# Performance work log

Hardware: AMD Instinct MI355X
Metric: run time of the kernel (lower is better)

## Reference

```python
import jax, jax.numpy as jnp
import numpy as np

NUM_GROUPS = 32
EPS = 1e-6


def setup_inputs() -> dict:
    key = jax.random.key(0)
    ks = jax.random.split(key, 11)
    b, c, h, w = 4, 512, 64, 64
    s = 0.02
    return {
        "x": jax.random.normal(ks[0], (b, c, h, w), dtype=jnp.float32),
        "gn_w": jnp.ones((c,), dtype=jnp.float32),
        "gn_b": jnp.zeros((c,), dtype=jnp.float32),
        "wq": jax.random.normal(ks[1], (c, c), dtype=jnp.float32) * s,
        "bq": jax.random.normal(ks[2], (c,), dtype=jnp.float32) * s,
        "wk": jax.random.normal(ks[3], (c, c), dtype=jnp.float32) * s,
        "bk": jax.random.normal(ks[4], (c,), dtype=jnp.float32) * s,
        "wv": jax.random.normal(ks[5], (c, c), dtype=jnp.float32) * s,
        "bv": jax.random.normal(ks[6], (c,), dtype=jnp.float32) * s,
        "wo": jax.random.normal(ks[7], (c, c), dtype=jnp.float32) * s,
        "bo": jax.random.normal(ks[8], (c,), dtype=jnp.float32) * s,
    }


def _group_norm(x, gamma, beta):
    b, c, h, w = x.shape
    g = NUM_GROUPS
    xg = x.reshape(b, g, c // g, h, w)
    mean = jnp.mean(xg, axis=(2, 3, 4), keepdims=True)
    var = jnp.var(xg, axis=(2, 3, 4), keepdims=True)
    xg = (xg - mean) * jax.lax.rsqrt(var + EPS)
    x = xg.reshape(b, c, h, w)
    return x * gamma[None, :, None, None] + beta[None, :, None, None]


def _conv1x1(x, wmat, bias):
    # x: [b,c,h,w], wmat: [out,in] -> [b,out,h,w]
    return jnp.einsum('bchw,oc->bohw', x, wmat) + bias[None, :, None, None]


def reference(x, gn_w, gn_b, wq, bq, wk, bk, wv, bv, wo, bo):
    b, c, h, w = x.shape
    h_ = _group_norm(x, gn_w, gn_b)
    q = _conv1x1(h_, wq, bq).reshape(b, c, h * w)  # [b,c,hw]
    k = _conv1x1(h_, wk, bk).reshape(b, c, h * w)
    v = _conv1x1(h_, wv, bv).reshape(b, c, h * w)
    scale = float(c) ** (-0.5)
    # scores[b,i,j] = sum_c q[b,c,i] * k[b,c,j]
    scores = jnp.einsum('bci,bcj->bij', q, k) * scale
    attn = jax.nn.softmax(scores, axis=2)  # softmax over j (keys)
    # out[b,c,i] = sum_j v[b,c,j] * attn[b,i,j]
    out = jnp.einsum('bcj,bij->bci', v, attn).reshape(b, c, h, w)
    out = _conv1x1(out, wo, bo)
    return x + out
```

## Files before the change

kernel.cpp:

```cpp
#include <hip/hip_runtime.h>
#include <math.h>

using short8 = __attribute__((ext_vector_type(8))) short;
using f32x4  = __attribute__((ext_vector_type(4))) float;
using llong2 = __attribute__((ext_vector_type(2))) long long;
using i32x8  = __attribute__((ext_vector_type(8))) int;

__device__ __forceinline__ ushort f2bf(float f) {
    union { float f; uint u; } c; c.f = f;
    uint u = c.u;
    uint r = (u + 0x7FFFu + ((u >> 16) & 1u)) >> 16;
    return (ushort)r;
}
__device__ __forceinline__ float bf2f(ushort h) {
    union { uint u; float f; } c; c.u = ((uint)h) << 16;
    return c.f;
}
__device__ __forceinline__ uint pk4_fp8(float a, float b, float c, float d) {
    int v = __builtin_amdgcn_cvt_pk_fp8_f32(a, b, 0, false);
    v = __builtin_amdgcn_cvt_pk_fp8_f32(c, d, v, true);
    return (uint)v;
}
__device__ __forceinline__ unsigned char f2fp8(float x) {
    return (unsigned char)__builtin_amdgcn_cvt_pk_fp8_f32(x, 0.f, 0, false);
}

__device__ __forceinline__ void gload16(const void* g, void* l) {
    __builtin_amdgcn_global_load_lds(
        (const __attribute__((address_space(1))) unsigned int*)g,
        (__attribute__((address_space(3))) unsigned int*)l,
        16, 0, 0);
}

__global__ __launch_bounds__(256) void prep_weights(
    const float* __restrict__ wq, const float* __restrict__ bq,
    const float* __restrict__ wk, const float* __restrict__ bk,
    const float* __restrict__ wv, const float* __restrict__ wo,
    ushort* __restrict__ Wqk, ushort* __restrict__ Wv, ushort* __restrict__ Wo,
    float* __restrict__ bqk, float* __restrict__ stats, float scale)
{
    int idx = blockIdx.x * 256 + threadIdx.x;
    if (idx < 1024 * 512) {
        float v = (idx < 262144) ? wq[idx] * scale : wk[idx - 262144];
        Wqk[idx] = f2bf(v);
    }
    if (idx < 262144) {
        Wv[idx] = f2bf(wv[idx]);
        Wo[idx] = f2bf(wo[idx]);
    }
    if (idx < 1024) bqk[idx] = (idx < 512) ? bq[idx] * scale : bk[idx - 512];
    if (idx < 256) stats[idx] = 0.f;
}

__global__ __launch_bounds__(256) void gn_stats(
    const float* __restrict__ x, float* __restrict__ stats)
{
    int blk = blockIdx.x;
    int grp = blk >> 3, sub = blk & 7;
    const float* xp = x + (size_t)grp * 65536 + sub * 8192;
    int tid = threadIdx.x;

    float s = 0.f, sq = 0.f;
    #pragma unroll
    for (int j = 0; j < 8; ++j) {
        float4 v = *(const float4*)&xp[tid * 4 + j * 1024];
        s  += v.x + v.y + v.z + v.w;
        sq += v.x * v.x + v.y * v.y + v.z * v.z + v.w * v.w;
    }
    #pragma unroll
    for (int off = 32; off; off >>= 1) {
        s  += __shfl_xor(s,  off, 64);
        sq += __shfl_xor(sq, off, 64);
    }
    __shared__ float red[8];
    if ((tid & 63) == 0) { red[(tid >> 6) * 2] = s; red[(tid >> 6) * 2 + 1] = sq; }
    __syncthreads();
    if (tid == 0) {
        atomicAdd(&stats[grp * 2],     red[0] + red[2] + red[4] + red[6]);
        atomicAdd(&stats[grp * 2 + 1], red[1] + red[3] + red[5] + red[7]);
    }
}

__global__ __launch_bounds__(256) void gn_apply(
    const float* __restrict__ x, const float* __restrict__ gamma,
    const float* __restrict__ beta, const float* __restrict__ stats,
    ushort* __restrict__ hnt)
{
    int blk = blockIdx.x;
    int grp = blk >> 4, tile = blk & 15;
    int b = grp >> 5, g = grp & 31;
    const float* xp = x + (size_t)grp * 65536;
    int tid = threadIdx.x;

    float mean = stats[grp * 2] * (1.f / 65536.f);
    float var  = stats[grp * 2 + 1] * (1.f / 65536.f) - mean * mean;
    float rstd = rsqrtf(var + 1e-6f);

    int i0 = tile * 256;
    __shared__ ushort ls[16][256];
    #pragma unroll
    for (int ch = 0; ch < 16; ++ch) {
        float a = rstd * gamma[g * 16 + ch];
        float c = beta[g * 16 + ch] - mean * a;
        ls[ch][tid] = f2bf(xp[ch * 4096 + i0 + tid] * a + c);
    }
    __syncthreads();
    ushort t[16];
    #pragma unroll
    for (int ch = 0; ch < 16; ++ch) t[ch] = ls[ch][tid];
    size_t dst = ((size_t)b * 4096 + i0 + tid) * 512 + g * 16;
    *(uint4*)&hnt[dst]     = *(const uint4*)&t[0];
    *(uint4*)&hnt[dst + 8] = *(const uint4*)&t[8];
}

__global__ __launch_bounds__(256) void softmax_kernel(
    const ushort* __restrict__ S, unsigned char* __restrict__ P8)
{
    size_t row = blockIdx.x;
    const ushort* p = S + row * 4096;
    int tid = threadIdx.x;

    ushort tmp[16];
    *(uint4*)&tmp[0] = *(const uint4*)&p[tid * 16];
    *(uint4*)&tmp[8] = *(const uint4*)&p[tid * 16 + 8];
    float v[16];
    float mx = -1e30f;
    #pragma unroll
    for (int j = 0; j < 16; ++j) { v[j] = bf2f(tmp[j]); mx = fmaxf(mx, v[j]); }
    #pragma unroll
    for (int off = 32; off; off >>= 1) mx = fmaxf(mx, __shfl_xor(mx, off, 64));
    __shared__ float ls[8];
    if ((tid & 63) == 0) ls[tid >> 6] = mx;
    __syncthreads();
    float m4 = fmaxf(fmaxf(ls[0], ls[1]), fmaxf(ls[2], ls[3]));
    float sum = 0.f;
    #pragma unroll
    for (int j = 0; j < 16; ++j) { v[j] = __expf(v[j] - m4); sum += v[j]; }
    #pragma unroll
    for (int off = 32; off; off >>= 1) sum += __shfl_xor(sum, off, 64);
    if ((tid & 63) == 0) ls[4 + (tid >> 6)] = sum;
    __syncthreads();
    float inv = 256.0f / (ls[4] + ls[5] + ls[6] + ls[7]);
    size_t base = row * 4096 + (size_t)tid * 16;
    uint2 o0, o1;
    o0.x = pk4_fp8(v[0] * inv,  v[1] * inv,  v[2] * inv,  v[3] * inv);
    o0.y = pk4_fp8(v[4] * inv,  v[5] * inv,  v[6] * inv,  v[7] * inv);
    o1.x = pk4_fp8(v[8] * inv,  v[9] * inv,  v[10] * inv, v[11] * inv);
    o1.y = pk4_fp8(v[12] * inv, v[13] * inv, v[14] * inv, v[15] * inv);
    *(uint2*)&P8[base]     = o0;
    *(uint2*)&P8[base + 8] = o1;
}

template <int BIAS, int OUT>
__global__ __launch_bounds__(256, 4) void gemm_nt(
    const ushort* __restrict__ Ag, const ushort* __restrict__ Bg,
    void* __restrict__ Cv, void* __restrict__ Cv2,
    const float* __restrict__ bias, const float* __restrict__ resid,
    int N, int K, int lda, int ldb,
    long sA, long sB, long sC)
{
    const int bz = blockIdx.z;
    Ag += (size_t)bz * sA;
    Bg += (size_t)bz * sB;

    const int tid  = threadIdx.x;
    const int wave = tid >> 6, lane = tid & 63;
    const int q = lane >> 4, lr = lane & 15;
    const int m0 = blockIdx.x * 128, n0 = blockIdx.y * 128;
    const int wm = (wave >> 1) * 64, wn = (wave & 1) * 64;

    __shared__ __align__(16) ushort As[2][128 * 32];
    __shared__ __align__(16) ushort Bs[2][128 * 32];

    const int srow = wave * 32 + (lane >> 2);
    const int skc  = (lane & 3) << 3;
    const size_t aoff0 = (size_t)(m0 + srow) * lda + skc;
    const size_t aoff1 = aoff0 + (size_t)16 * lda;
    const size_t boff0 = (size_t)(n0 + srow) * ldb + skc;
    const size_t boff1 = boff0 + (size_t)16 * ldb;
    const int l0 = wave * 1024, l1 = wave * 1024 + 512;

    f32x4 acc[4][4] = {};

    for (int kb = 0; kb < K; kb += 64) {
        __syncthreads();
        gload16(&Ag[aoff0 + kb],      &As[0][l0]);
        gload16(&Ag[aoff1 + kb],      &As[0][l1]);
        gload16(&Ag[aoff0 + kb + 32], &As[1][l0]);
        gload16(&Ag[aoff1 + kb + 32], &As[1][l1]);
        gload16(&Bg[boff0 + kb],      &Bs[0][l0]);
        gload16(&Bg[boff1 + kb],      &Bs[0][l1]);
        gload16(&Bg[boff0 + kb + 32], &Bs[1][l0]);
        gload16(&Bg[boff1 + kb + 32], &Bs[1][l1]);
        __syncthreads();

        #pragma unroll
        for (int kh = 0; kh < 2; ++kh) {
            short8 af[4], bfr[4];
            #pragma unroll
            for (int mt = 0; mt < 4; ++mt)
                af[mt] = *(const short8*)&As[kh][(wm + mt * 16 + lr) * 32 + q * 8];
            #pragma unroll
            for (int nt = 0; nt < 4; ++nt)
                bfr[nt] = *(const short8*)&Bs[kh][(wn + nt * 16 + lr) * 32 + q * 8];
            #pragma unroll
            for (int mt = 0; mt < 4; ++mt)
                #pragma unroll
                for (int nt = 0; nt < 4; ++nt)
                    acc[mt][nt] = __builtin_amdgcn_mfma_f32_16x16x32_bf16(
                        af[mt], bfr[nt], acc[mt][nt], 0, 0, 0);
        }
    }

    if (OUT == 2 || OUT == 3) {
        __syncthreads();
        unsigned char* C8 = (unsigned char*)&As[0][0];
        #pragma unroll
        for (int mt = 0; mt < 4; ++mt) {
            #pragma unroll
            for (int nt = 0; nt < 4; ++nt) {
                int col = wn + nt * 16 + lr;
                #pragma unroll
                for (int t = 0; t < 4; ++t) {
                    int row = wm + mt * 16 + q * 4 + t;
                    float v = acc[mt][nt][t];
                    if (BIAS == 1) v += bias[m0 + row];
                    if (BIAS == 2) v += bias[n0 + col];
                    if (OUT == 3 && n0 < 512) v *= 16.f;
                    C8[row * 128 + ((((col >> 4) ^ (row & 7)) << 4) | (col & 15))]
                        = f2fp8(v);
                }
            }
        }
        __syncthreads();
        const int er = tid >> 3, eck = tid & 7;
        #pragma unroll
        for (int p = 0; p < 4; ++p) {
            int row = p * 32 + er;
            uint4 v = *(const uint4*)&C8[row * 128 + ((eck ^ (row & 7)) << 4)];
            if (OUT == 2) {
                *(uint4*)&((unsigned char*)Cv)[(size_t)bz * sC
                    + (size_t)(m0 + row) * N + n0 + eck * 16] = v;
            } else {
                if (n0 < 512)
                    *(uint4*)&((unsigned char*)Cv)[(size_t)bz * sC
                        + (size_t)(m0 + row) * 512 + n0 + eck * 16] = v;
                else
                    *(uint4*)&((unsigned char*)Cv2)[(size_t)bz * sC
                        + (size_t)(m0 + row) * 512 + (n0 - 512) + eck * 16] = v;
            }
        }
        return;
    }

    #pragma unroll
    for (int mt = 0; mt < 4; ++mt) {
        int rb = m0 + wm + mt * 16 + q * 4;
        #pragma unroll
        for (int nt = 0; nt < 4; ++nt) {
            int cn = n0 + wn + nt * 16 + lr;
            #pragma unroll
            for (int t = 0; t < 4; ++t) {
                int r = rb + t;
                float v = acc[mt][nt][t];
                if (BIAS == 1) v += bias[r];
                if (BIAS == 2) v += bias[cn];
                if (OUT == 1) {
                    size_t o = (size_t)bz * sC + (size_t)r * N + cn;
                    ((float*)Cv)[o] = v + resid[o];
                } else {
                    size_t o = (size_t)bz * sC + (size_t)r * N + cn;
                    ((ushort*)Cv)[o] = f2bf(v);
                }
            }
        }
    }
}

__global__ __launch_bounds__(256, 2) void gemm_qk(
    const unsigned char* __restrict__ Q8, const unsigned char* __restrict__ K8,
    ushort* __restrict__ S)
{
    const int bz = blockIdx.z;
    const unsigned char* Ag = Q8 + (size_t)bz * 2097152;
    const unsigned char* Bg = K8 + (size_t)bz * 2097152;

    const int tid  = threadIdx.x;
    const int wave = tid >> 6, lane = tid & 63;
    const int q = lane >> 4, lr = lane & 15;
    const int m0 = blockIdx.x * 128, n0 = blockIdx.y * 128;
    const int wm = (wave >> 1) * 64, wn = (wave & 1) * 64;

    __shared__ __align__(16) unsigned char smem[32768];
    unsigned char* As = smem;
    unsigned char* Bs = smem + 16384;
    ushort* Cs = (ushort*)smem;

    const int lrow = lane >> 3;
    const size_t laneoff = (size_t)lrow * 512 + ((lane & 7) ^ (lrow & 7)) * 16;
    const size_t abase = (size_t)(m0 + wave * 32) * 512 + laneoff;
    const size_t bbase = (size_t)(n0 + wave * 32) * 512 + laneoff;
    unsigned char* lA = As + wave * 32 * 128;
    unsigned char* lB = Bs + wave * 32 * 128;

    const int e0 = (2 * q) ^ (lr & 7), e1 = e0 ^ 1;

    f32x4 acc[4][4] = {};
    const int sA = 0x7B7B7B7B;
    const int sB = 0x7F7F7F7F;

    for (int kb = 0; kb < 512; kb += 128) {
        __syncthreads();
        #pragma unroll
        for (int t = 0; t < 4; ++t) {
            gload16(Ag + abase + (size_t)t * 4096 + kb, lA + t * 1024);
            gload16(Bg + bbase + (size_t)t * 4096 + kb, lB + t * 1024);
        }
        __syncthreads();

        i32x8 af[4], bf[4];
        #pragma unroll
        for (int mt = 0; mt < 4; ++mt) {
            int r = wm + mt * 16 + lr;
            union { uint4 v[2]; i32x8 f; } u;
            u.v[0] = *(const uint4*)&As[r * 128 + e0 * 16];
            u.v[1] = *(const uint4*)&As[r * 128 + e1 * 16];
            af[mt] = u.f;
        }
        #pragma unroll
        for (int nt = 0; nt < 4; ++nt) {
            int r = wn + nt * 16 + lr;
            union { uint4 v[2]; i32x8 f; } u;
            u.v[0] = *(const uint4*)&Bs[r * 128 + e0 * 16];
            u.v[1] = *(const uint4*)&Bs[r * 128 + e1 * 16];
            bf[nt] = u.f;
        }
        #pragma unroll
        for (int mt = 0; mt < 4; ++mt)
            #pragma unroll
            for (int nt = 0; nt < 4; ++nt)
                acc[mt][nt] = __builtin_amdgcn_mfma_scale_f32_16x16x128_f8f6f4(
                    af[mt], bf[nt], acc[mt][nt], 0, 0, 0, sA, 0, sB);
    }

    __syncthreads();
    #pragma unroll
    for (int mt = 0; mt < 4; ++mt) {
        #pragma unroll
        for (int nt = 0; nt < 4; ++nt) {
            int col = wn + nt * 16 + lr;
            #pragma unroll
            for (int t = 0; t < 4; ++t) {
                int row = wm + mt * 16 + q * 4 + t;
                Cs[row * 128 + ((((col >> 3) ^ (row & 7)) << 3) | (col & 7))]
                    = f2bf(acc[mt][nt][t]);
            }
        }
    }
    __syncthreads();
    const int er = tid >> 4, eck = tid & 15;
    ushort* orow = S + (size_t)bz * 16777216 + (size_t)m0 * 4096 + n0;
    #pragma unroll
    for (int p = 0; p < 8; ++p) {
        int row = p * 16 + er;
        uint4 v = *(const uint4*)&Cs[row * 128 + ((eck ^ (row & 7)) << 3)];
        *(uint4*)&orow[(size_t)row * 4096 + eck * 8] = v;
    }
}

__global__ __launch_bounds__(256, 2) void gemm_pv(
    const unsigned char* __restrict__ P8, const unsigned char* __restrict__ V8,
    ushort* __restrict__ Ot)
{
    const int bz = blockIdx.z;
    const unsigned char* Ag = P8 + (size_t)bz * 16777216;
    const unsigned char* Bg = V8 + (size_t)bz * 2097152;

    const int tid  = threadIdx.x;
    const int wave = tid >> 6, lane = tid & 63;
    const int q = lane >> 4, lr = lane & 15;
    const int m0 = blockIdx.x * 128, n0 = blockIdx.y * 128;
    const int wm = (wave >> 1) * 64, wn = (wave & 1) * 64;

    __shared__ __align__(16) unsigned char smem[32768];
    unsigned char* As = smem;
    unsigned char* Bs = smem + 16384;
    ushort* Cs = (ushort*)smem;

    const int lrow = lane >> 3;
    const size_t laneoff = (size_t)lrow * 4096 + ((lane & 7) ^ (lrow & 7)) * 16;
    const size_t abase = (size_t)(m0 + wave * 32) * 4096 + laneoff;
    const size_t bbase = (size_t)(n0 + wave * 32) * 4096 + laneoff;
    unsigned char* lA = As + wave * 32 * 128;
    unsigned char* lB = Bs + wave * 32 * 128;

    const int e0 = (2 * q) ^ (lr & 7), e1 = e0 ^ 1;

    f32x4 acc[4][4] = {};
    const int sA = 0x77777777;
    const int sB = 0x7F7F7F7F;

    for (int kb = 0; kb < 4096; kb += 128) {
        __syncthreads();
        #pragma unroll
        for (int t = 0; t < 4; ++t) {
            gload16(Ag + abase + (size_t)t * 32768 + kb, lA + t * 1024);
            gload16(Bg + bbase + (size_t)t * 32768 + kb, lB + t * 1024);
        }
        __syncthreads();

        i32x8 af[4], bf[4];
        #pragma unroll
        for (int mt = 0; mt < 4; ++mt) {
            int r = wm + mt * 16 + lr;
            union { uint4 v[2]; i32x8 f; } u;
            u.v[0] = *(const uint4*)&As[r * 128 + e0 * 16];
            u.v[1] = *(const uint4*)&As[r * 128 + e1 * 16];
            af[mt] = u.f;
        }
        #pragma unroll
        for (int nt = 0; nt < 4; ++nt) {
            int r = wn + nt * 16 + lr;
            union { uint4 v[2]; i32x8 f; } u;
            u.v[0] = *(const uint4*)&Bs[r * 128 + e0 * 16];
            u.v[1] = *(const uint4*)&Bs[r * 128 + e1 * 16];
            bf[nt] = u.f;
        }
        #pragma unroll
        for (int mt = 0; mt < 4; ++mt)
            #pragma unroll
            for (int nt = 0; nt < 4; ++nt)
                acc[mt][nt] = __builtin_amdgcn_mfma_scale_f32_16x16x128_f8f6f4(
                    af[mt], bf[nt], acc[mt][nt], 0, 0, 0, sA, 0, sB);
    }

    __syncthreads();
    #pragma unroll
    for (int mt = 0; mt < 4; ++mt) {
        #pragma unroll
        for (int nt = 0; nt < 4; ++nt) {
            int col = wn + nt * 16 + lr;
            #pragma unroll
            for (int t = 0; t < 4; ++t) {
                int row = wm + mt * 16 + q * 4 + t;
                Cs[row * 128 + ((((col >> 3) ^ (row & 7)) << 3) | (col & 7))]
                    = f2bf(acc[mt][nt][t]);
            }
        }
    }
    __syncthreads();
    const int er = tid >> 4, eck = tid & 15;
    ushort* orow = Ot + (size_t)bz * 2097152 + (size_t)m0 * 512 + n0;
    #pragma unroll
    for (int p = 0; p < 8; ++p) {
        int row = p * 16 + er;
        uint4 v = *(const uint4*)&Cs[row * 128 + ((eck ^ (row & 7)) << 3)];
        *(uint4*)&orow[(size_t)row * 512 + eck * 8] = v;
    }
}

extern "C" void kernel_launch(void* const* d_in, const int* in_sizes, int n_in,
                              void* d_out, int out_size, void* d_ws, size_t ws_size,
                              hipStream_t stream)
{
    const float* x   = (const float*)d_in[0];
    const float* gnw = (const float*)d_in[1];
    const float* gnb = (const float*)d_in[2];
    const float* wq  = (const float*)d_in[3];
    const float* bq  = (const float*)d_in[4];
    const float* wk  = (const float*)d_in[5];
    const float* bk  = (const float*)d_in[6];
    const float* wv  = (const float*)d_in[7];
    const float* bv  = (const float*)d_in[8];
    const float* wo  = (const float*)d_in[9];
    const float* bo  = (const float*)d_in[10];
    float* out = (float*)d_out;

    char* ws = (char*)d_ws;
    ushort*        S   = (ushort*)(ws);
    ushort*        Ot  = (ushort*)(ws);
    ushort*        hnt = (ushort*)(ws + 134217728);
    unsigned char* Q8  = (unsigned char*)(ws + 150994944);
    unsigned char* K8  = (unsigned char*)(ws + 159383552);
    unsigned char* P8  = (unsigned char*)(ws + 134217728);
    unsigned char* V8  = (unsigned char*)(ws + 201326592);
    ushort*        Wqk = (ushort*)(ws + 209715200);
    ushort*        Wv  = (ushort*)(ws + 210763776);
    ushort*        Wo  = (ushort*)(ws + 211288064);
    float*         bqk = (float*) (ws + 211812352);
    float*         st  = (float*) (ws + 211816448);

    const float scale = 1.0f / sqrtf(512.0f);
    const long sHW  = 512L * 4096;

    prep_weights<<<2048, 256, 0, stream>>>(wq, bq, wk, bk, wv, wo,
                                           Wqk, Wv, Wo, bqk, st, scale);
    gn_stats<<<1024, 256, 0, stream>>>(x, st);
    gn_apply<<<2048, 256, 0, stream>>>(x, gnw, gnb, st, hnt);

    gemm_nt<2, 3><<<dim3(32, 8, 4), 256, 0, stream>>>(
        hnt, Wqk, Q8, K8, bqk, nullptr,
        1024, 512, 512, 512, sHW, 0L, sHW);

    gemm_nt<1, 2><<<dim3(4, 32, 4), 256, 0, stream>>>(
        Wv, hnt, V8, nullptr, bv, nullptr,
        4096, 512, 512, 512, 0L, sHW, sHW);

    gemm_qk<<<dim3(32, 32, 4), 256, 0, stream>>>(Q8, K8, S);

    softmax_kernel<<<16384, 256, 0, stream>>>(S, P8);

    gemm_pv<<<dim3(32, 4, 4), 256, 0, stream>>>(P8, V8, Ot);

    gemm_nt<1, 1><<<dim3(4, 32, 4), 256, 0, stream>>>(
        Wo, Ot, out, nullptr, bo, x,
        4096, 512, 512, 512, 0L, sHW, sHW);
}
```

Measured before the change: 285.5 us.

## Double-buffer LDS tiles in QK and PV fp8 GEMMs with prefetch pipelining

```diff
diff --git a/kernel.cpp b/kernel.cpp
--- a/kernel.cpp
+++ b/kernel.cpp
@@ -291,17 +291,15 @@
     const int m0 = blockIdx.x * 128, n0 = blockIdx.y * 128;
     const int wm = (wave >> 1) * 64, wn = (wave & 1) * 64;
 
-    __shared__ __align__(16) unsigned char smem[32768];
-    unsigned char* As = smem;
-    unsigned char* Bs = smem + 16384;
-    ushort* Cs = (ushort*)smem;
+    __shared__ __align__(16) unsigned char As[2][16384];
+    __shared__ __align__(16) unsigned char Bs[2][16384];
+    ushort* Cs = (ushort*)&As[0][0];
 
     const int lrow = lane >> 3;
     const size_t laneoff = (size_t)lrow * 512 + ((lane & 7) ^ (lrow & 7)) * 16;
     const size_t abase = (size_t)(m0 + wave * 32) * 512 + laneoff;
     const size_t bbase = (size_t)(n0 + wave * 32) * 512 + laneoff;
-    unsigned char* lA = As + wave * 32 * 128;
-    unsigned char* lB = Bs + wave * 32 * 128;
+    const int lws = wave * 4096;
 
     const int e0 = (2 * q) ^ (lr & 7), e1 = e0 ^ 1;
 
@@ -309,41 +307,60 @@
     const int sA = 0x7B7B7B7B;
     const int sB = 0x7F7F7F7F;
 
-    for (int kb = 0; kb < 512; kb += 128) {
-        __syncthreads();
+    auto stage = [&](int kb, unsigned char* dA, unsigned char* dB) {
         #pragma unroll
         for (int t = 0; t < 4; ++t) {
-            gload16(Ag + abase + (size_t)t * 4096 + kb, lA + t * 1024);
-            gload16(Bg + bbase + (size_t)t * 4096 + kb, lB + t * 1024);
-        }
-        __syncthreads();
-
+            gload16(Ag + abase + (size_t)t * 4096 + kb, dA + lws + t * 1024);
+            gload16(Bg + bbase + (size_t)t * 4096 + kb, dB + lws + t * 1024);
+        }
+    };
+    auto compute = [&](const unsigned char* cA, const unsigned char* cB) {
         i32x8 af[4], bf[4];
         #pragma unroll
         for (int mt = 0; mt < 4; ++mt) {
             int r = wm + mt * 16 + lr;
             union { uint4 v[2]; i32x8 f; } u;
-            u.v[0] = *(const uint4*)&As[r * 128 + e0 * 16];
-            u.v[1] = *(const uint4*)&As[r * 128 + e1 * 16];
+            u.v[0] = *(const uint4*)&cA[r * 128 + e0 * 16];
+            u.v[1] = *(const uint4*)&cA[r * 128 + e1 * 16];
             af[mt] = u.f;
         }
         #pragma unroll
         for (int nt = 0; nt < 4; ++nt) {
             int r = wn + nt * 16 + lr;
             union { uint4 v[2]; i32x8 f; } u;
-            u.v[0] = *(const uint4*)&Bs[r * 128 + e0 * 16];
-            u.v[1] = *(const uint4*)&Bs[r * 128 + e1 * 16];
+            u.v[0] = *(const uint4*)&cB[r * 128 + e0 * 16];
+            u.v[1] = *(const uint4*)&cB[r * 128 + e1 * 16];
             bf[nt] = u.f;
         }
+        __builtin_amdgcn_s_setprio(1);
         #pragma unroll
         for (int mt = 0; mt < 4; ++mt)
             #pragma unroll
             for (int nt = 0; nt < 4; ++nt)
                 acc[mt][nt] = __builtin_amdgcn_mfma_scale_f32_16x16x128_f8f6f4(
                     af[mt], bf[nt], acc[mt][nt], 0, 0, 0, sA, 0, sB);
-    }
-
-    __syncthreads();
+        __builtin_amdgcn_s_setprio(0);
+    };
+
+    stage(0, As[0], Bs[0]);
+    #pragma unroll
+    for (int it = 0; it < 4; ++it) {
+        const int cur = it & 1;
+        if (it < 3) {
+            stage((it + 1) * 128, As[cur ^ 1], Bs[cur ^ 1]);
+            asm volatile("s_waitcnt vmcnt(8)" ::: "memory");
+        } else {
+            asm volatile("s_waitcnt vmcnt(0)" ::: "memory");
+        }
+        __builtin_amdgcn_s_barrier();
+        __builtin_amdgcn_sched_barrier(0);
+        compute(As[cur], Bs[cur]);
+        asm volatile("s_waitcnt lgkmcnt(0)" ::: "memory");
+        __builtin_amdgcn_sched_barrier(0);
+        __builtin_amdgcn_s_barrier();
+        __builtin_amdgcn_sched_barrier(0);
+    }
+
     #pragma unroll
     for (int mt = 0; mt < 4; ++mt) {
         #pragma unroll
@@ -382,17 +399,15 @@
     const int m0 = blockIdx.x * 128, n0 = blockIdx.y * 128;
     const int wm = (wave >> 1) * 64, wn = (wave & 1) * 64;
 
-    __shared__ __align__(16) unsigned char smem[32768];
-    unsigned char* As = smem;
-    unsigned char* Bs = smem + 16384;
-    ushort* Cs = (ushort*)smem;
+    __shared__ __align__(16) unsigned char As[2][16384];
+    __shared__ __align__(16) unsigned char Bs[2][16384];
+    ushort* Cs = (ushort*)&As[0][0];
 
     const int lrow = lane >> 3;
     const size_t laneoff = (size_t)lrow * 4096 + ((lane & 7) ^ (lrow & 7)) * 16;
     const size_t abase = (size_t)(m0 + wave * 32) * 4096 + laneoff;
     const size_t bbase = (size_t)(n0 + wave * 32) * 4096 + laneoff;
-    unsigned char* lA = As + wave * 32 * 128;
-    unsigned char* lB = Bs + wave * 32 * 128;
+    const int lws = wave * 4096;
 
     const int e0 = (2 * q) ^ (lr & 7), e1 = e0 ^ 1;
 
@@ -400,41 +415,67 @@
     const int sA = 0x77777777;
     const int sB = 0x7F7F7F7F;
 
-    for (int kb = 0; kb < 4096; kb += 128) {
-        __syncthreads();
+    auto stage = [&](int kb, unsigned char* dA, unsigned char* dB) {
         #pragma unroll
         for (int t = 0; t < 4; ++t) {
-            gload16(Ag + abase + (size_t)t * 32768 + kb, lA + t * 1024);
-            gload16(Bg + bbase + (size_t)t * 32768 + kb, lB + t * 1024);
-        }
-        __syncthreads();
-
+            gload16(Ag + abase + (size_t)t * 32768 + kb, dA + lws + t * 1024);
+            gload16(Bg + bbase + (size_t)t * 32768 + kb, dB + lws + t * 1024);
+        }
+    };
+    auto compute = [&](const unsigned char* cA, const unsigned char* cB) {
         i32x8 af[4], bf[4];
         #pragma unroll
         for (int mt = 0; mt < 4; ++mt) {
             int r = wm + mt * 16 + lr;
             union { uint4 v[2]; i32x8 f; } u;
-            u.v[0] = *(const uint4*)&As[r * 128 + e0 * 16];
-            u.v[1] = *(const uint4*)&As[r * 128 + e1 * 16];
+            u.v[0] = *(const uint4*)&cA[r * 128 + e0 * 16];
+            u.v[1] = *(const uint4*)&cA[r * 128 + e1 * 16];
             af[mt] = u.f;
         }
         #pragma unroll
         for (int nt = 0; nt < 4; ++nt) {
             int r = wn + nt * 16 + lr;
             union { uint4 v[2]; i32x8 f; } u;
-            u.v[0] = *(const uint4*)&Bs[r * 128 + e0 * 16];
-            u.v[1] = *(const uint4*)&Bs[r * 128 + e1 * 16];
+            u.v[0] = *(const uint4*)&cB[r * 128 + e0 * 16];
+            u.v[1] = *(const uint4*)&cB[r * 128 + e1 * 16];
             bf[nt] = u.f;
         }
+        __builtin_amdgcn_s_setprio(1);
         #pragma unroll
         for (int mt = 0; mt < 4; ++mt)
             #pragma unroll
             for (int nt = 0; nt < 4; ++nt)
                 acc[mt][nt] = __builtin_amdgcn_mfma_scale_f32_16x16x128_f8f6f4(
                     af[mt], bf[nt], acc[mt][nt], 0, 0, 0, sA, 0, sB);
-    }
-
-    __syncthreads();
+        __builtin_amdgcn_s_setprio(0);
+    };
+
+    stage(0, As[0], Bs[0]);
+    for (int it2 = 0; it2 < 32; it2 += 2) {
+        stage((it2 + 1) * 128, As[1], Bs[1]);
+        asm volatile("s_waitcnt vmcnt(8)" ::: "memory");
+        __builtin_amdgcn_s_barrier();
+        __builtin_amdgcn_sched_barrier(0);
+        compute(As[0], Bs[0]);
+        asm volatile("s_waitcnt lgkmcnt(0)" ::: "memory");
+        __builtin_amdgcn_sched_barrier(0);
+        __builtin_amdgcn_s_barrier();
+        __builtin_amdgcn_sched_barrier(0);
+        if (it2 + 2 < 32) {
+            stage((it2 + 2) * 128, As[0], Bs[0]);
+            asm volatile("s_waitcnt vmcnt(8)" ::: "memory");
+        } else {
+            asm volatile("s_waitcnt vmcnt(0)" ::: "memory");
+        }
+        __builtin_amdgcn_s_barrier();
+        __builtin_amdgcn_sched_barrier(0);
+        compute(As[1], Bs[1]);
+        asm volatile("s_waitcnt lgkmcnt(0)" ::: "memory");
+        __builtin_amdgcn_sched_barrier(0);
+        __builtin_amdgcn_s_barrier();
+        __builtin_amdgcn_sched_barrier(0);
+    }
+
     #pragma unroll
     for (int mt = 0; mt < 4; ++mt) {
         #pragma unroll
```

New measurement: 294.9 us. 3.3% more time.
